# Optimization experiments

Measured on AMD Instinct MI355X. Metric: run time of the kernel, lower is better.

## Reference

```python
import jax, jax.numpy as jnp
import numpy as np

WS = 16            # window height = width
DIM = 512          # channels
H = 16             # num heads
HD = DIM // H      # head dim = 32
NW = 64            # num windows per image (mask leading dim)
B_ = 256           # num_windows * batch
N_IN = 512         # pre-stride sequence length
SCALE = HD ** -0.5
MAX_SEQ = 512
STRIDE = 2


def _relative_position_index(wh, ww):
    coords = np.stack(np.meshgrid(np.arange(wh), np.arange(ww), indexing='ij'))  # (2, wh, ww)
    cf = coords.reshape(2, -1)                             # (2, wh*ww)
    rc = (cf[:, :, None] - cf[:, None, :]).transpose(1, 2, 0).astype(np.int32)
    rc[:, :, 0] += wh - 1
    rc[:, :, 1] += ww - 1
    rc[:, :, 0] *= 2 * ww - 1
    return rc.sum(-1)                                      # (wh*ww, wh*ww)


def setup_inputs() -> dict:
    key = jax.random.key(0)
    ks = jax.random.split(key, 8)
    x = jax.random.normal(ks[0], (B_, N_IN, DIM), dtype=jnp.float32)
    y = jax.random.normal(ks[1], (B_, N_IN, DIM), dtype=jnp.float32)
    mask = jax.random.normal(ks[2], (NW, WS * WS, WS * WS), dtype=jnp.float32)
    q_w = jax.random.normal(ks[3], (DIM, DIM), dtype=jnp.float32) * 0.02
    q_b = jnp.zeros((DIM,), dtype=jnp.float32)
    kv_w = jax.random.normal(ks[4], (2 * DIM, DIM), dtype=jnp.float32) * 0.02
    kv_b = jnp.zeros((2 * DIM,), dtype=jnp.float32)
    proj_w = jax.random.normal(ks[5], (DIM, DIM), dtype=jnp.float32) * 0.02
    proj_b = jnp.zeros((DIM,), dtype=jnp.float32)
    bias_table = jax.random.normal(ks[6], ((2 * WS - 1) ** 2, H), dtype=jnp.float32) * 0.02
    rel_pos_index = jnp.asarray(_relative_position_index(WS, WS))  # (256, 256) int32
    return {"x": x, "y": y, "mask": mask, "q_w": q_w, "q_b": q_b,
            "kv_w": kv_w, "kv_b": kv_b, "proj_w": proj_w, "proj_b": proj_b,
            "bias_table": bias_table, "rel_pos_index": rel_pos_index}


def reference(x, y, mask, q_w, q_b, kv_w, kv_b, proj_w, proj_b, bias_table, rel_pos_index):
    # truncate + stride (as in forward)
    x = x[:, :MAX_SEQ][:, ::STRIDE]          # (B_, N, C), N = 256
    y = y[:, :MAX_SEQ][:, ::STRIDE]
    b, n, c = x.shape
    # projections
    q = (x @ q_w.T + q_b).reshape(b, n, H, HD).transpose(0, 2, 1, 3)   # (B_, H, N, D)
    kv = y @ kv_w.T + kv_b                                              # (B_, N, 2C)
    k = kv[..., :DIM].reshape(b, n, H, HD).transpose(0, 2, 1, 3)
    v = kv[..., DIM:].reshape(b, n, H, HD).transpose(0, 2, 1, 3)
    # scores
    attn = jnp.einsum('bhnd,bhmd->bhnm', q * SCALE, k)                  # (B_, H, N, N)
    # gathered relative position bias: (N, N, H) -> (H, N, N)
    rpb = bias_table[rel_pos_index].transpose(2, 0, 1)
    attn = attn + rpb[None]
    # window mask: view (B_//nW, nW, H, N, N) + mask[None,:,None]
    attn = attn.reshape(b // NW, NW, H, n, n) + mask[None, :, None]
    attn = attn.reshape(b, H, n, n)
    attn = jax.nn.softmax(attn, axis=-1)
    out = jnp.einsum('bhnm,bhmd->bhnd', attn, v)                        # (B_, H, N, D)
    out = out.transpose(0, 2, 1, 3).reshape(b, n, DIM)
    out = out @ proj_w.T + proj_b
    return out
```

## Files before the change

kernel.cpp:

```cpp
#include <hip/hip_runtime.h>

typedef _Float16 half8 __attribute__((ext_vector_type(8)));
typedef _Float16 half4 __attribute__((ext_vector_type(4)));
typedef _Float16 half2v __attribute__((ext_vector_type(2)));
typedef float f32x4 __attribute__((ext_vector_type(4)));

#define LOG2E 1.4426950408889634f
#define QSCALE (0.17677669529663687f * 1.4426950408889634f)

static __device__ __forceinline__ half4 cvt4h(float4 v) {
    half2v a = __builtin_bit_cast(half2v, __builtin_amdgcn_cvt_pkrtz(v.x, v.y));
    half2v b = __builtin_bit_cast(half2v, __builtin_amdgcn_cvt_pkrtz(v.z, v.w));
    return half4{ a[0], a[1], b[0], b[1] };
}

#define NB_X 16384
#define NB_Y 16384
#define NB_W 512
#define NB_M 4096
#define NB_R 4096

__global__ __launch_bounds__(256) void convert_kernel(
    const float* __restrict__ x, const float* __restrict__ y,
    const float* __restrict__ q_w, const float* __restrict__ kv_w,
    const float* __restrict__ proj_w, const float* __restrict__ mask,
    const float* __restrict__ table, const int* __restrict__ rpi,
    _Float16* __restrict__ Xh, _Float16* __restrict__ Yh,
    _Float16* __restrict__ Wh, _Float16* __restrict__ maskh,
    _Float16* __restrict__ rpbh)
{
    const int blk = blockIdx.x, t = threadIdx.x;
    if (blk < NB_X + NB_Y) {
        const float* src; _Float16* dst; int v;
        if (blk < NB_X) { v = blk * 256 + t; src = x; dst = Xh; }
        else { v = (blk - NB_X) * 256 + t; src = y; dst = Yh; }
        int r = v >> 6, ks = (v & 63) * 8;
        const float* s = src + ((size_t)(r >> 8) * 512 + (size_t)((r & 255) * 2)) * 512 + ks;
        half4 h0 = cvt4h(*(const float4*)s);
        half4 h1 = cvt4h(*(const float4*)(s + 4));
        half8 hv = { h0[0], h0[1], h0[2], h0[3], h1[0], h1[1], h1[2], h1[3] };
        *(half8*)(dst + (size_t)v * 8) = hv;
    } else if (blk < NB_X + NB_Y + NB_W) {
        int v = (blk - NB_X - NB_Y) * 256 + t;
        int row = v >> 6, ks = (v & 63) * 8;
        const float* s; float sc = 1.0f;
        if (row < 512)       { s = q_w + (size_t)row * 512;            sc = QSCALE; }
        else if (row < 1536) { s = kv_w + (size_t)(row - 512) * 512; }
        else                 { s = proj_w + (size_t)(row - 1536) * 512; }
        float4 a = *(const float4*)(s + ks);
        float4 b = *(const float4*)(s + ks + 4);
        a.x *= sc; a.y *= sc; a.z *= sc; a.w *= sc;
        b.x *= sc; b.y *= sc; b.z *= sc; b.w *= sc;
        half4 h0 = cvt4h(a), h1 = cvt4h(b);
        half8 hv = { h0[0], h0[1], h0[2], h0[3], h1[0], h1[1], h1[2], h1[3] };
        *(half8*)(Wh + (size_t)v * 8) = hv;
    } else if (blk < NB_X + NB_Y + NB_W + NB_M) {
        int i = (blk - NB_X - NB_Y - NB_W) * 256 + t;
        float4 v = ((const float4*)mask)[i];
        half4 hv = { (_Float16)(v.x * LOG2E), (_Float16)(v.y * LOG2E),
                     (_Float16)(v.z * LOG2E), (_Float16)(v.w * LOG2E) };
        *(half4*)(maskh + (size_t)i * 4) = hv;
    } else {
        int i = (blk - NB_X - NB_Y - NB_W - NB_M) * 256 + t;
        int p = i & 65535, hh = i >> 16;
        rpbh[i] = (_Float16)(table[rpi[p] * 16 + hh] * LOG2E);
    }
}

__global__ __launch_bounds__(256) void gemm_f16(
    const _Float16* __restrict__ Ah, const _Float16* __restrict__ Wh,
    const float* __restrict__ bias, float bscale,
    _Float16* __restrict__ qout, _Float16* __restrict__ kout,
    _Float16* __restrict__ vout, float* __restrict__ fout,
    int mode, int nct_sh)
{
    __shared__ __align__(16) _Float16 As[128 * 64];
    __shared__ __align__(16) _Float16 Ws[128 * 64];
    const int nwg = gridDim.x;
    const int chunk = nwg >> 3;
    const int f = blockIdx.x;
    const int swz = (f & 7) * chunk + (f >> 3);
    const int ct = swz & ((1 << nct_sh) - 1);
    const int rt = swz >> nct_sh;

    const int t = threadIdx.x;
    const int lane = t & 63, wave = t >> 6;
    const int ql = lane & 15, g = lane >> 4;
    const int wr = (wave >> 1) * 64, wc = (wave & 1) * 64;

    const int sr = t >> 3;
    const int st = t & 7;
    const _Float16* aR = Ah + ((size_t)(rt * 128 + sr)) * 512 + st * 8;
    const _Float16* wR = Wh + ((size_t)(ct * 128 + sr)) * 512 + st * 8;
    char* asw = (char*)As + sr * 128 + ((st ^ (sr & 7)) << 4);
    char* wsw = (char*)Ws + sr * 128 + ((st ^ (sr & 7)) << 4);

    f32x4 acc[4][4] = {};
    for (int kk = 0; kk < 8; ++kk) {
        const int k0 = kk * 64;
        half8 a0 = *(const half8*)(aR + k0);
        half8 a1 = *(const half8*)(aR + 32 * 512 + k0);
        half8 a2 = *(const half8*)(aR + 64 * 512 + k0);
        half8 a3 = *(const half8*)(aR + 96 * 512 + k0);
        half8 w0 = *(const half8*)(wR + k0);
        half8 w1 = *(const half8*)(wR + 32 * 512 + k0);
        half8 w2 = *(const half8*)(wR + 64 * 512 + k0);
        half8 w3 = *(const half8*)(wR + 96 * 512 + k0);
        if (kk) __syncthreads();
        *(half8*)(asw)           = a0;
        *(half8*)(asw + 32*128)  = a1;
        *(half8*)(asw + 64*128)  = a2;
        *(half8*)(asw + 96*128)  = a3;
        *(half8*)(wsw)           = w0;
        *(half8*)(wsw + 32*128)  = w1;
        *(half8*)(wsw + 64*128)  = w2;
        *(half8*)(wsw + 96*128)  = w3;
        __syncthreads();
#pragma unroll
        for (int kh = 0; kh < 2; ++kh) {
            half8 af[4], bf[4];
#pragma unroll
            for (int i = 0; i < 4; ++i) {
                int row = wr + i * 16 + ql;
                af[i] = *(const half8*)((const char*)As + row * 128 +
                        (((kh * 4 + g) ^ (ql & 7)) << 4));
            }
#pragma unroll
            for (int j = 0; j < 4; ++j) {
                int row = wc + j * 16 + ql;
                bf[j] = *(const half8*)((const char*)Ws + row * 128 +
                        (((kh * 4 + g) ^ (ql & 7)) << 4));
            }
#pragma unroll
            for (int i = 0; i < 4; ++i)
#pragma unroll
                for (int j = 0; j < 4; ++j)
                    acc[i][j] = __builtin_amdgcn_mfma_f32_16x16x32_f16(af[i], bf[j], acc[i][j], 0, 0, 0);
        }
    }

#pragma unroll
    for (int j = 0; j < 4; ++j) {
        int c = ct * 128 + wc + j * 16 + ql;
        float bv = bias[c] * bscale;
#pragma unroll
        for (int i = 0; i < 4; ++i) {
#pragma unroll
            for (int rr = 0; rr < 4; ++rr) {
                int r = rt * 128 + wr + i * 16 + g * 4 + rr;
                float val = acc[i][j][rr] + bv;
                if (mode == 2) {
                    fout[(size_t)r * 512 + c] = val;
                } else {
                    _Float16 hv = (_Float16)val;
                    int b = r >> 8, n = r & 255;
                    if (mode == 0) {
                        int hh = c >> 5, d = c & 31;
                        qout[((size_t)(b * 16 + hh) * 256 + n) * 32 + d] = hv;
                    } else if (c < 512) {
                        int hh = c >> 5, d = c & 31;
                        kout[((size_t)(b * 16 + hh) * 256 + n) * 32 + d] = hv;
                    } else {
                        int c2 = c - 512, hh = c2 >> 5, d = c2 & 31;
                        vout[((size_t)(b * 16 + hh) * 256 + n) * 32 + d] = hv;
                    }
                }
            }
        }
    }
}

__global__ __launch_bounds__(256, 2) void attn_kernel(
    const _Float16* __restrict__ Q, const _Float16* __restrict__ K,
    const _Float16* __restrict__ V, const _Float16* __restrict__ rpbh,
    const _Float16* __restrict__ maskh, _Float16* __restrict__ pre)
{
    __shared__ __align__(16) _Float16 bias_s[2][16 * 256];
    const int blk = blockIdx.x;
    const int w = blk >> 4, h = blk & 15;
    const int t = threadIdx.x;
    const int lane = t & 63, wave = t >> 6;
    const int ql = lane & 15, g = lane >> 4;
    const int b = w + 64 * wave;
    const size_t blk_b = (size_t)(b * 16 + h) * 8192;
    const _Float16* Qp = Q + blk_b + g * 8;
    const _Float16* Kp = K + blk_b + ql * 32 + g * 8;
    const _Float16* rp = rpbh + (size_t)h * 65536;
    const _Float16* mp = maskh + (size_t)w * 65536;

    half8 karr[16];
#pragma unroll
    for (int tt = 0; tt < 16; ++tt)
        karr[tt] = *(const half8*)(Kp + tt * 512);

    half4 vf0[16], vf1[16];
    {
        const _Float16* vb = V + blk_b + g * 128 + ql;
#pragma unroll
        for (int tt = 0; tt < 16; ++tt) {
#pragma unroll
            for (int j = 0; j < 4; ++j) {
                vf0[tt][j] = vb[tt * 512 + j * 32];
                vf1[tt][j] = vb[tt * 512 + j * 32 + 16];
            }
        }
    }

    const int sq = t >> 4;
    const int scb = (t & 15) * 32;
    const int sw = sq << 3;
    const int sgoff = (t & 15) * 16;

    {
        const _Float16* rrow = rp + (size_t)sq * 256 + sgoff;
        const _Float16* mrow = mp + (size_t)sq * 256 + sgoff;
        half8 s0 = *(const half8*)rrow + *(const half8*)mrow;
        half8 s1 = *(const half8*)(rrow + 8) + *(const half8*)(mrow + 8);
        char* sb = (char*)bias_s[0] + sq * 512;
        *(half4*)(sb + ((scb) ^ sw))      = __builtin_shufflevector(s0, s0, 0, 1, 2, 3);
        *(half4*)(sb + ((scb + 8) ^ sw))  = __builtin_shufflevector(s0, s0, 4, 5, 6, 7);
        *(half4*)(sb + ((scb + 16) ^ sw)) = __builtin_shufflevector(s1, s1, 0, 1, 2, 3);
        *(half4*)(sb + ((scb + 24) ^ sw)) = __builtin_shufflevector(s1, s1, 4, 5, 6, 7);
    }
    __syncthreads();

#pragma unroll 1
    for (int qg = 0; qg < 16; ++qg) {
        const int q0 = qg * 16;
        half8 nr0, nm0, nr1, nm1;
        if (qg < 15) {
            const _Float16* rrow = rp + (size_t)(q0 + 16 + sq) * 256 + sgoff;
            const _Float16* mrow = mp + (size_t)(q0 + 16 + sq) * 256 + sgoff;
            nr0 = *(const half8*)rrow;
            nm0 = *(const half8*)mrow;
            nr1 = *(const half8*)(rrow + 8);
            nm1 = *(const half8*)(mrow + 8);
        }

        const int q = q0 + ql;
        half8 qf = *(const half8*)(Qp + (size_t)q * 32);
        const char* bb = (const char*)bias_s[qg & 1] + ql * 512;
        f32x4 lsum = { 0.f, 0.f, 0.f, 0.f };
        f32x4 o0 = { 0.f, 0.f, 0.f, 0.f }, o1 = { 0.f, 0.f, 0.f, 0.f };
#pragma unroll
        for (int tt = 0; tt < 16; ++tt) {
            half4 bs = *(const half4*)(bb + ((tt * 32 + g * 8) ^ (ql << 3)));
            f32x4 bf = { (float)bs[0], (float)bs[1], (float)bs[2], (float)bs[3] };
            f32x4 s = __builtin_amdgcn_mfma_f32_16x16x32_f16(karr[tt], qf, bf, 0, 0, 0);
            float e0 = __builtin_amdgcn_exp2f(s[0]);
            float e1 = __builtin_amdgcn_exp2f(s[1]);
            float e2 = __builtin_amdgcn_exp2f(s[2]);
            float e3 = __builtin_amdgcn_exp2f(s[3]);
            lsum[0] += e0; lsum[1] += e1; lsum[2] += e2; lsum[3] += e3;
            half2v p01 = __builtin_bit_cast(half2v, __builtin_amdgcn_cvt_pkrtz(e0, e1));
            half2v p23 = __builtin_bit_cast(half2v, __builtin_amdgcn_cvt_pkrtz(e2, e3));
            half4 pf = { p01[0], p01[1], p23[0], p23[1] };
            o0 = __builtin_amdgcn_mfma_f32_16x16x16f16(pf, vf0[tt], o0, 0, 0, 0);
            o1 = __builtin_amdgcn_mfma_f32_16x16x16f16(pf, vf1[tt], o1, 0, 0, 0);
        }
        float l = (lsum[0] + lsum[1]) + (lsum[2] + lsum[3]);
        l += __shfl_xor(l, 16);
        l += __shfl_xor(l, 32);
#pragma unroll
        for (int rr = 0; rr < 4; ++rr) {
            float inv = __builtin_amdgcn_rcpf(__shfl(l, g * 4 + rr));
            int row = q0 + g * 4 + rr;
            size_t ob = ((size_t)b * 256 + row) * 512 + h * 32;
            pre[ob + ql] = (_Float16)(o0[rr] * inv);
            pre[ob + 16 + ql] = (_Float16)(o1[rr] * inv);
        }
        if (qg < 15) {
            half8 s0 = nr0 + nm0, s1 = nr1 + nm1;
            char* sb = (char*)bias_s[(qg + 1) & 1] + sq * 512;
            *(half4*)(sb + ((scb) ^ sw))      = __builtin_shufflevector(s0, s0, 0, 1, 2, 3);
            *(half4*)(sb + ((scb + 8) ^ sw))  = __builtin_shufflevector(s0, s0, 4, 5, 6, 7);
            *(half4*)(sb + ((scb + 16) ^ sw)) = __builtin_shufflevector(s1, s1, 0, 1, 2, 3);
            *(half4*)(sb + ((scb + 24) ^ sw)) = __builtin_shufflevector(s1, s1, 4, 5, 6, 7);
        }
        __syncthreads();
    }
}

extern "C" void kernel_launch(void* const* d_in, const int* in_sizes, int n_in,
                              void* d_out, int out_size, void* d_ws, size_t ws_size,
                              hipStream_t stream)
{
    const float* x      = (const float*)d_in[0];
    const float* y      = (const float*)d_in[1];
    const float* mask   = (const float*)d_in[2];
    const float* q_w    = (const float*)d_in[3];
    const float* q_b    = (const float*)d_in[4];
    const float* kv_w   = (const float*)d_in[5];
    const float* kv_b   = (const float*)d_in[6];
    const float* proj_w = (const float*)d_in[7];
    const float* proj_b = (const float*)d_in[8];
    const float* btab   = (const float*)d_in[9];
    const int*   rpi    = (const int*)d_in[10];
    float* out = (float*)d_out;

    char* ws = (char*)d_ws;
    _Float16* XK  = (_Float16*)(ws);
    _Float16* YP  = (_Float16*)(ws + ((size_t)64 << 20));
    _Float16* Qw  = (_Float16*)(ws + ((size_t)128 << 20));
    _Float16* Vw  = (_Float16*)(ws + ((size_t)192 << 20));
    _Float16* Wh  = (_Float16*)(ws + ((size_t)256 << 20));
    _Float16* Rpb = (_Float16*)(ws + ((size_t)258 << 20));
    _Float16* Mh  = (_Float16*)(ws + ((size_t)260 << 20));

    convert_kernel<<<NB_X + NB_Y + NB_W + NB_M + NB_R, 256, 0, stream>>>(
        x, y, q_w, kv_w, proj_w, mask, btab, rpi, XK, YP, Wh, Mh, Rpb);
    gemm_f16<<<2048, 256, 0, stream>>>(XK, Wh, q_b, QSCALE,
                                       Qw, nullptr, nullptr, nullptr, 0, 2);
    gemm_f16<<<4096, 256, 0, stream>>>(YP, Wh + 512 * 512, kv_b, 1.0f,
                                       nullptr, XK, Vw, nullptr, 1, 3);
    attn_kernel<<<1024, 256, 0, stream>>>(Qw, XK, Vw, Rpb, Mh, YP);
    gemm_f16<<<2048, 256, 0, stream>>>(YP, Wh + 1536 * 512, proj_b, 1.0f,
                                       nullptr, nullptr, nullptr, out, 2, 2);
}
```

Measured before the change: 501.2 us.

## Widen GEMM tile to 128x256 and prefetch next K-slice into registers

The projection GEMM tile grows from 128x128 to 128x256 output columns, so each wave now computes a 64x128 sub-tile with 32 accumulators. The grids are halved to match. Global loads for the next K-step are issued right after the shared-memory barrier and held in registers, overlapping them with the MFMA work. The aim is less redundant A-tile traffic and hidden global-load latency, paid for with more registers and shared memory, which may lower occupancy.

```diff
diff --git a/kernel.cpp b/kernel.cpp
--- a/kernel.cpp
+++ b/kernel.cpp
@@ -75,7 +75,7 @@
     int mode, int nct_sh)
 {
     __shared__ __align__(16) _Float16 As[128 * 64];
-    __shared__ __align__(16) _Float16 Ws[128 * 64];
+    __shared__ __align__(16) _Float16 Ws[256 * 64];
     const int nwg = gridDim.x;
     const int chunk = nwg >> 3;
     const int f = blockIdx.x;
@@ -86,62 +86,79 @@
     const int t = threadIdx.x;
     const int lane = t & 63, wave = t >> 6;
     const int ql = lane & 15, g = lane >> 4;
-    const int wr = (wave >> 1) * 64, wc = (wave & 1) * 64;
+    const int wr = (wave >> 1) * 64, wc = (wave & 1) * 128;
 
     const int sr = t >> 3;
     const int st = t & 7;
     const _Float16* aR = Ah + ((size_t)(rt * 128 + sr)) * 512 + st * 8;
-    const _Float16* wR = Wh + ((size_t)(ct * 128 + sr)) * 512 + st * 8;
+    const _Float16* wR = Wh + ((size_t)(ct * 256 + sr)) * 512 + st * 8;
     char* asw = (char*)As + sr * 128 + ((st ^ (sr & 7)) << 4);
     char* wsw = (char*)Ws + sr * 128 + ((st ^ (sr & 7)) << 4);
 
-    f32x4 acc[4][4] = {};
+    half8 sA0 = *(const half8*)(aR);
+    half8 sA1 = *(const half8*)(aR + 32 * 512);
+    half8 sA2 = *(const half8*)(aR + 64 * 512);
+    half8 sA3 = *(const half8*)(aR + 96 * 512);
+    half8 sW0 = *(const half8*)(wR);
+    half8 sW1 = *(const half8*)(wR + 32 * 512);
+    half8 sW2 = *(const half8*)(wR + 64 * 512);
+    half8 sW3 = *(const half8*)(wR + 96 * 512);
+    half8 sW4 = *(const half8*)(wR + 128 * 512);
+    half8 sW5 = *(const half8*)(wR + 160 * 512);
+    half8 sW6 = *(const half8*)(wR + 192 * 512);
+    half8 sW7 = *(const half8*)(wR + 224 * 512);
+
+    f32x4 acc[4][8] = {};
     for (int kk = 0; kk < 8; ++kk) {
-        const int k0 = kk * 64;
-        half8 a0 = *(const half8*)(aR + k0);
-        half8 a1 = *(const half8*)(aR + 32 * 512 + k0);
-        half8 a2 = *(const half8*)(aR + 64 * 512 + k0);
-        half8 a3 = *(const half8*)(aR + 96 * 512 + k0);
-        half8 w0 = *(const half8*)(wR + k0);
-        half8 w1 = *(const half8*)(wR + 32 * 512 + k0);
-        half8 w2 = *(const half8*)(wR + 64 * 512 + k0);
-        half8 w3 = *(const half8*)(wR + 96 * 512 + k0);
         if (kk) __syncthreads();
-        *(half8*)(asw)           = a0;
-        *(half8*)(asw + 32*128)  = a1;
-        *(half8*)(asw + 64*128)  = a2;
-        *(half8*)(asw + 96*128)  = a3;
-        *(half8*)(wsw)           = w0;
-        *(half8*)(wsw + 32*128)  = w1;
-        *(half8*)(wsw + 64*128)  = w2;
-        *(half8*)(wsw + 96*128)  = w3;
+        *(half8*)(asw)            = sA0;
+        *(half8*)(asw + 32*128)   = sA1;
+        *(half8*)(asw + 64*128)   = sA2;
+        *(half8*)(asw + 96*128)   = sA3;
+        *(half8*)(wsw)            = sW0;
+        *(half8*)(wsw + 32*128)   = sW1;
+        *(half8*)(wsw + 64*128)   = sW2;
+        *(half8*)(wsw + 96*128)   = sW3;
+        *(half8*)(wsw + 128*128)  = sW4;
+        *(half8*)(wsw + 160*128)  = sW5;
+        *(half8*)(wsw + 192*128)  = sW6;
+        *(half8*)(wsw + 224*128)  = sW7;
         __syncthreads();
+        if (kk < 7) {
+            const int k0n = (kk + 1) * 64;
+            sA0 = *(const half8*)(aR + k0n);
+            sA1 = *(const half8*)(aR + 32 * 512 + k0n);
+            sA2 = *(const half8*)(aR + 64 * 512 + k0n);
+            sA3 = *(const half8*)(aR + 96 * 512 + k0n);
+            sW0 = *(const half8*)(wR + k0n);
+            sW1 = *(const half8*)(wR + 32 * 512 + k0n);
+            sW2 = *(const half8*)(wR + 64 * 512 + k0n);
+            sW3 = *(const half8*)(wR + 96 * 512 + k0n);
+            sW4 = *(const half8*)(wR + 128 * 512 + k0n);
+            sW5 = *(const half8*)(wR + 160 * 512 + k0n);
+            sW6 = *(const half8*)(wR + 192 * 512 + k0n);
+            sW7 = *(const half8*)(wR + 224 * 512 + k0n);
+        }
 #pragma unroll
         for (int kh = 0; kh < 2; ++kh) {
-            half8 af[4], bf[4];
-#pragma unroll
-            for (int i = 0; i < 4; ++i) {
-                int row = wr + i * 16 + ql;
-                af[i] = *(const half8*)((const char*)As + row * 128 +
-                        (((kh * 4 + g) ^ (ql & 7)) << 4));
+            const int so = ((kh * 4 + g) ^ (ql & 7)) << 4;
+            half8 af[4];
+#pragma unroll
+            for (int i = 0; i < 4; ++i)
+                af[i] = *(const half8*)((const char*)As + (wr + i * 16 + ql) * 128 + so);
+#pragma unroll
+            for (int j = 0; j < 8; ++j) {
+                half8 bf = *(const half8*)((const char*)Ws + (wc + j * 16 + ql) * 128 + so);
+#pragma unroll
+                for (int i = 0; i < 4; ++i)
+                    acc[i][j] = __builtin_amdgcn_mfma_f32_16x16x32_f16(af[i], bf, acc[i][j], 0, 0, 0);
             }
-#pragma unroll
-            for (int j = 0; j < 4; ++j) {
-                int row = wc + j * 16 + ql;
-                bf[j] = *(const half8*)((const char*)Ws + row * 128 +
-                        (((kh * 4 + g) ^ (ql & 7)) << 4));
-            }
-#pragma unroll
-            for (int i = 0; i < 4; ++i)
-#pragma unroll
-                for (int j = 0; j < 4; ++j)
-                    acc[i][j] = __builtin_amdgcn_mfma_f32_16x16x32_f16(af[i], bf[j], acc[i][j], 0, 0, 0);
-        }
-    }
-
-#pragma unroll
-    for (int j = 0; j < 4; ++j) {
-        int c = ct * 128 + wc + j * 16 + ql;
+        }
+    }
+
+#pragma unroll
+    for (int j = 0; j < 8; ++j) {
+        int c = ct * 256 + wc + j * 16 + ql;
         float bv = bias[c] * bscale;
 #pragma unroll
         for (int i = 0; i < 4; ++i) {
@@ -309,11 +326,11 @@
 
     convert_kernel<<<NB_X + NB_Y + NB_W + NB_M + NB_R, 256, 0, stream>>>(
         x, y, q_w, kv_w, proj_w, mask, btab, rpi, XK, YP, Wh, Mh, Rpb);
-    gemm_f16<<<2048, 256, 0, stream>>>(XK, Wh, q_b, QSCALE,
-                                       Qw, nullptr, nullptr, nullptr, 0, 2);
-    gemm_f16<<<4096, 256, 0, stream>>>(YP, Wh + 512 * 512, kv_b, 1.0f,
-                                       nullptr, XK, Vw, nullptr, 1, 3);
+    gemm_f16<<<1024, 256, 0, stream>>>(XK, Wh, q_b, QSCALE,
+                                       Qw, nullptr, nullptr, nullptr, 0, 1);
+    gemm_f16<<<2048, 256, 0, stream>>>(YP, Wh + 512 * 512, kv_b, 1.0f,
+                                       nullptr, XK, Vw, nullptr, 1, 2);
     attn_kernel<<<1024, 256, 0, stream>>>(Qw, XK, Vw, Rpb, Mh, YP);
-    gemm_f16<<<2048, 256, 0, stream>>>(YP, Wh + 1536 * 512, proj_b, 1.0f,
-                                       nullptr, nullptr, nullptr, out, 2, 2);
-}
+    gemm_f16<<<1024, 256, 0, stream>>>(YP, Wh + 1536 * 512, proj_b, 1.0f,
+                                       nullptr, nullptr, nullptr, out, 2, 1);
+}
```

New measurement: 577.2 us. +15.2%, slower.
